# Kernel optimization log

Measured on AMD Instinct MI355X. Metric: run time of the kernel, lower is better.

The kernel has to match this reference:

```python
import jax, jax.numpy as jnp
import numpy as np

EMBED_DIM = 2048
HIDDEN_DIM = 2048
SEQ_LEN = 8192


def setup_inputs() -> dict:
    key = jax.random.key(0)
    ks = jax.random.split(key, 6)
    x = jax.random.normal(ks[0], (SEQ_LEN, EMBED_DIM), dtype=jnp.float32)
    # original uses torch.rand (uniform [0,1)) for params
    W_h = jax.random.uniform(ks[1], (HIDDEN_DIM, HIDDEN_DIM), dtype=jnp.float32)
    W_x = jax.random.uniform(ks[2], (HIDDEN_DIM, EMBED_DIM), dtype=jnp.float32)
    W_y = jax.random.uniform(ks[3], (EMBED_DIM, HIDDEN_DIM), dtype=jnp.float32)
    B_h = jax.random.uniform(ks[4], (HIDDEN_DIM,), dtype=jnp.float32)
    B_y = jax.random.uniform(ks[5], (EMBED_DIM,), dtype=jnp.float32)
    return {"x": x, "W_h": W_h, "W_x": W_x, "W_y": W_y, "B_h": B_h, "B_y": B_y}


def reference(x, W_h, W_x, W_y, B_h, B_y):
    # Precompute input projections for all timesteps in one GEMM: [T, H]
    xp = x @ W_x.T + B_h

    def step(h, xp_t):
        h_new = jnp.tanh(W_h @ h + xp_t)  # [H]
        return h_new, h_new

    h0 = jnp.zeros((W_h.shape[0],), dtype=x.dtype)
    h_final, hs = jax.lax.scan(step, h0, xp)  # hs: [T, H]
    # Output projection + softmax over embed dim, batched over timesteps
    logits = hs @ W_y.T + B_y  # [T, E]
    output = jax.nn.softmax(logits, axis=-1)
    return (h_final, output)
```

## Files before the change

kernel.cpp:

```cpp
#include <hip/hip_runtime.h>

#define T_SEQ 8192
#define HDIM  2048
#define EDIM  2048
#define RBLK  64
#define ROWS_PER_BLK (HDIM / RBLK)

typedef unsigned long long u64;
typedef __attribute__((ext_vector_type(4))) unsigned int u32x4;
typedef __attribute__((ext_vector_type(4))) float f32x4;

__device__ inline void poll_pair(const u64* p0, const u64* p1, u32x4& a, u32x4& b) {
    asm volatile("global_load_dwordx4 %0, %2, off sc1\n\t"
                 "global_load_dwordx4 %1, %3, off sc1\n\t"
                 "s_waitcnt vmcnt(0)"
                 : "=v"(a), "=v"(b) : "v"(p0), "v"(p1) : "memory");
}

__device__ inline f32x4 ld_w16(const float* p) {
    f32x4 r;
    asm volatile("global_load_dwordx4 %0, %1, off" : "=v"(r) : "v"(p));
    return r;
}

__device__ inline float fast_tanh(float z) {
    float zc = fminf(fmaxf(z, -15.f), 15.f);
    float zs = zc * 2.88539008177792681f;
    float ez; asm("v_exp_f32 %0, %1" : "=v"(ez) : "v"(zs));
    float rc; float ezp = ez + 1.f;
    asm("v_rcp_f32 %0, %1" : "=v"(rc) : "v"(ezp));
    return (ez - 1.f) * rc;
}

__global__ __launch_bounds__(256) void gemm128_nt_bias(
    const float* __restrict__ A, const float* __restrict__ B,
    const float* __restrict__ bias, float* __restrict__ C,
    int M, int N, int K)
{
    __shared__ float As[16][128 + 4];
    __shared__ float Bs[16][128 + 4];

    const int tid = threadIdx.x;
    const int tx = tid & 15;
    const int ty = tid >> 4;
    const int m0 = blockIdx.y * 128;
    const int n0 = blockIdx.x * 128;

    float acc[8][8] = {};

    for (int kk = 0; kk < K; kk += 16) {
        #pragma unroll
        for (int p = 0; p < 2; ++p) {
            int idx = p * 256 + tid;
            int r  = idx >> 2;
            int cb = (idx & 3) * 4;
            float4 va = *(const float4*)&A[(size_t)(m0 + r) * K + kk + cb];
            As[cb + 0][r] = va.x; As[cb + 1][r] = va.y;
            As[cb + 2][r] = va.z; As[cb + 3][r] = va.w;
            float4 vb = *(const float4*)&B[(size_t)(n0 + r) * K + kk + cb];
            Bs[cb + 0][r] = vb.x; Bs[cb + 1][r] = vb.y;
            Bs[cb + 2][r] = vb.z; Bs[cb + 3][r] = vb.w;
        }
        __syncthreads();
        #pragma unroll
        for (int k = 0; k < 16; ++k) {
            float4 a0 = *(const float4*)&As[k][ty * 8];
            float4 a1 = *(const float4*)&As[k][ty * 8 + 4];
            float4 b0 = *(const float4*)&Bs[k][tx * 8];
            float4 b1 = *(const float4*)&Bs[k][tx * 8 + 4];
            float av[8] = {a0.x, a0.y, a0.z, a0.w, a1.x, a1.y, a1.z, a1.w};
            float bv[8] = {b0.x, b0.y, b0.z, b0.w, b1.x, b1.y, b1.z, b1.w};
            #pragma unroll
            for (int i = 0; i < 8; ++i)
                #pragma unroll
                for (int j = 0; j < 8; ++j)
                    acc[i][j] = fmaf(av[i], bv[j], acc[i][j]);
        }
        __syncthreads();
    }

    float4 bb0 = *(const float4*)&bias[n0 + tx * 8];
    float4 bb1 = *(const float4*)&bias[n0 + tx * 8 + 4];
    float bv[8] = {bb0.x, bb0.y, bb0.z, bb0.w, bb1.x, bb1.y, bb1.z, bb1.w};
    #pragma unroll
    for (int i = 0; i < 8; ++i) {
        float4 o0, o1;
        o0.x = acc[i][0] + bv[0]; o0.y = acc[i][1] + bv[1];
        o0.z = acc[i][2] + bv[2]; o0.w = acc[i][3] + bv[3];
        o1.x = acc[i][4] + bv[4]; o1.y = acc[i][5] + bv[5];
        o1.z = acc[i][6] + bv[6]; o1.w = acc[i][7] + bv[7];
        float* cp = &C[(size_t)(m0 + ty * 8 + i) * N + n0 + tx * 8];
        *(float4*)cp = o0;
        *(float4*)(cp + 4) = o1;
    }
}

__global__ __launch_bounds__(256) void gemm128_nt_bias_tc(
    const float* __restrict__ A, const float* __restrict__ B,
    const float* __restrict__ bias, float* __restrict__ Ct,
    int M, int N, int K)
{
    __shared__ float As[16][128 + 4];
    __shared__ float Bs[16][128 + 4];

    const int tid = threadIdx.x;
    const int tx = tid & 15;
    const int ty = tid >> 4;
    const int m0 = blockIdx.y * 128;
    const int n0 = blockIdx.x * 128;

    float acc[8][8] = {};

    for (int kk = 0; kk < K; kk += 16) {
        #pragma unroll
        for (int p = 0; p < 2; ++p) {
            int idx = p * 256 + tid;
            int r  = idx >> 2;
            int cb = (idx & 3) * 4;
            float4 va = *(const float4*)&A[(size_t)(m0 + r) * K + kk + cb];
            As[cb + 0][r] = va.x; As[cb + 1][r] = va.y;
            As[cb + 2][r] = va.z; As[cb + 3][r] = va.w;
            float4 vb = *(const float4*)&B[(size_t)(n0 + r) * K + kk + cb];
            Bs[cb + 0][r] = vb.x; Bs[cb + 1][r] = vb.y;
            Bs[cb + 2][r] = vb.z; Bs[cb + 3][r] = vb.w;
        }
        __syncthreads();
        #pragma unroll
        for (int k = 0; k < 16; ++k) {
            float4 a0 = *(const float4*)&As[k][ty * 8];
            float4 a1 = *(const float4*)&As[k][ty * 8 + 4];
            float4 b0 = *(const float4*)&Bs[k][tx * 8];
            float4 b1 = *(const float4*)&Bs[k][tx * 8 + 4];
            float av[8] = {a0.x, a0.y, a0.z, a0.w, a1.x, a1.y, a1.z, a1.w};
            float bv[8] = {b0.x, b0.y, b0.z, b0.w, b1.x, b1.y, b1.z, b1.w};
            #pragma unroll
            for (int i = 0; i < 8; ++i)
                #pragma unroll
                for (int j = 0; j < 8; ++j)
                    acc[i][j] = fmaf(av[i], bv[j], acc[i][j]);
        }
        __syncthreads();
    }

    #pragma unroll
    for (int j = 0; j < 8; ++j) {
        float bb = bias[n0 + tx * 8 + j];
        float4 o0, o1;
        o0.x = acc[0][j] + bb; o0.y = acc[1][j] + bb;
        o0.z = acc[2][j] + bb; o0.w = acc[3][j] + bb;
        o1.x = acc[4][j] + bb; o1.y = acc[5][j] + bb;
        o1.z = acc[6][j] + bb; o1.w = acc[7][j] + bb;
        float* cp = &Ct[(size_t)(n0 + tx * 8 + j) * M + m0 + ty * 8];
        *(float4*)cp = o0;
        *(float4*)(cp + 4) = o1;
    }
}

__global__ __launch_bounds__(512, 1) void rnn_recurrence(
    const float* __restrict__ Wh, const float* __restrict__ xpT,
    float* __restrict__ Hs, u64* __restrict__ hbuf, int T)
{
    const int tid  = threadIdx.x;
    const int lane = tid & 63;
    const int wid  = tid >> 6;
    const int r0   = blockIdx.x * ROWS_PER_BLK + wid * 4;

    const float* wr0 = Wh + (size_t)(r0 + 0) * HDIM + lane * 4;
    const float* wr1 = Wh + (size_t)(r0 + 1) * HDIM + lane * 4;
    const float* wr2 = Wh + (size_t)(r0 + 2) * HDIM + lane * 4;
    const float* wr3 = Wh + (size_t)(r0 + 3) * HDIM + lane * 4;

    f32x4 w00 = ld_w16(wr0 + 0*256), w01 = ld_w16(wr0 + 1*256), w02 = ld_w16(wr0 + 2*256), w03 = ld_w16(wr0 + 3*256);
    f32x4 w04 = ld_w16(wr0 + 4*256), w05 = ld_w16(wr0 + 5*256), w06 = ld_w16(wr0 + 6*256), w07 = ld_w16(wr0 + 7*256);
    f32x4 w10 = ld_w16(wr1 + 0*256), w11 = ld_w16(wr1 + 1*256), w12 = ld_w16(wr1 + 2*256), w13 = ld_w16(wr1 + 3*256);
    f32x4 w14 = ld_w16(wr1 + 4*256), w15 = ld_w16(wr1 + 5*256), w16 = ld_w16(wr1 + 6*256), w17 = ld_w16(wr1 + 7*256);
    f32x4 w20 = ld_w16(wr2 + 0*256), w21 = ld_w16(wr2 + 1*256), w22 = ld_w16(wr2 + 2*256), w23 = ld_w16(wr2 + 3*256);
    f32x4 w24 = ld_w16(wr2 + 4*256), w25 = ld_w16(wr2 + 5*256), w26 = ld_w16(wr2 + 6*256), w27 = ld_w16(wr2 + 7*256);
    f32x4 w30 = ld_w16(wr3 + 0*256), w31 = ld_w16(wr3 + 1*256), w32 = ld_w16(wr3 + 2*256), w33 = ld_w16(wr3 + 3*256);
    f32x4 w34 = ld_w16(wr3 + 4*256), w35 = ld_w16(wr3 + 5*256), w36 = ld_w16(wr3 + 6*256), w37 = ld_w16(wr3 + 7*256);
    asm volatile("s_waitcnt vmcnt(0)" ::: "memory");

    __shared__ float hsm[HDIM];

    for (int t = 0; t < T; ++t) {
        float xq = 0.f;
        if (lane < 4) xq = xpT[(size_t)(r0 + lane) * T + t];

        float sv = 0.f;
        if (t > 0) {
            const u64* hb = hbuf + (size_t)(t & 1) * HDIM;
            const unsigned tg = (unsigned)t;
            const u64* p0 = hb + 2 * tid;
            const u64* p1 = hb + 1024 + 2 * tid;

            u32x4 a, b;
            poll_pair(p0, p1, a, b);
            while ((a.y != tg) | (a.w != tg) | (b.y != tg) | (b.w != tg))
                poll_pair(p0, p1, a, b);

            ((float2*)hsm)[tid] =
                make_float2(__uint_as_float(a.x), __uint_as_float(a.z));
            ((float2*)hsm)[tid + 512] =
                make_float2(__uint_as_float(b.x), __uint_as_float(b.z));
            __syncthreads();

            float s0 = 0.f, s1 = 0.f, s2 = 0.f, s3 = 0.f;
            #define RNN_STEP(IDX, WA, WB, WC, WD)                                   \
            {   float4 h4 = ((const float4*)hsm)[(IDX) * 64 + lane];                \
                s0 = fmaf(WA.x, h4.x, s0); s0 = fmaf(WA.y, h4.y, s0);               \
                s0 = fmaf(WA.z, h4.z, s0); s0 = fmaf(WA.w, h4.w, s0);               \
                s1 = fmaf(WB.x, h4.x, s1); s1 = fmaf(WB.y, h4.y, s1);               \
                s1 = fmaf(WB.z, h4.z, s1); s1 = fmaf(WB.w, h4.w, s1);               \
                s2 = fmaf(WC.x, h4.x, s2); s2 = fmaf(WC.y, h4.y, s2);               \
                s2 = fmaf(WC.z, h4.z, s2); s2 = fmaf(WC.w, h4.w, s2);               \
                s3 = fmaf(WD.x, h4.x, s3); s3 = fmaf(WD.y, h4.y, s3);               \
                s3 = fmaf(WD.z, h4.z, s3); s3 = fmaf(WD.w, h4.w, s3); }
            RNN_STEP(0, w00, w10, w20, w30)
            RNN_STEP(1, w01, w11, w21, w31)
            RNN_STEP(2, w02, w12, w22, w32)
            RNN_STEP(3, w03, w13, w23, w33)
            RNN_STEP(4, w04, w14, w24, w34)
            RNN_STEP(5, w05, w15, w25, w35)
            RNN_STEP(6, w06, w16, w26, w36)
            RNN_STEP(7, w07, w17, w27, w37)
            #undef RNN_STEP

            float fa = (lane & 1) ? s1 : s0;
            float fb = (lane & 1) ? s0 : s1;
            fa += __shfl_xor(fb, 1);
            float fc = (lane & 1) ? s3 : s2;
            float fd = (lane & 1) ? s2 : s3;
            fc += __shfl_xor(fd, 1);
            float fe = (lane & 2) ? fc : fa;
            float ff = (lane & 2) ? fa : fc;
            fe += __shfl_xor(ff, 2);
            #pragma unroll
            for (int off = 4; off < 64; off <<= 1) fe += __shfl_xor(fe, off);
            sv = fe;
        }

        if (lane < 4) {
            float hn = fast_tanh(sv + xq);
            u64 pk = ((u64)(unsigned)(t + 1) << 32) | (u64)__float_as_uint(hn);
            (void)__hip_atomic_exchange(
                &hbuf[(size_t)((t + 1) & 1) * HDIM + r0 + lane], pk,
                __ATOMIC_RELAXED, __HIP_MEMORY_SCOPE_AGENT);
            Hs[(size_t)t * HDIM + r0 + lane] = hn;
        }
    }
}

__global__ __launch_bounds__(256) void softmax_rows(
    const float* __restrict__ logits, float* __restrict__ out)
{
    const int row = blockIdx.x;
    const float4* in4 = (const float4*)(logits + (size_t)row * EDIM);
    float4* out4 = (float4*)(out + (size_t)row * EDIM);

    float4 v0 = in4[threadIdx.x];
    float4 v1 = in4[threadIdx.x + 256];

    float m = fmaxf(fmaxf(fmaxf(v0.x, v0.y), fmaxf(v0.z, v0.w)),
                    fmaxf(fmaxf(v1.x, v1.y), fmaxf(v1.z, v1.w)));
    #pragma unroll
    for (int off = 32; off > 0; off >>= 1) m = fmaxf(m, __shfl_xor(m, off));

    __shared__ float red[4];
    if ((threadIdx.x & 63) == 0) red[threadIdx.x >> 6] = m;
    __syncthreads();
    m = fmaxf(fmaxf(red[0], red[1]), fmaxf(red[2], red[3]));
    __syncthreads();

    float e[8];
    e[0] = expf(v0.x - m); e[1] = expf(v0.y - m);
    e[2] = expf(v0.z - m); e[3] = expf(v0.w - m);
    e[4] = expf(v1.x - m); e[5] = expf(v1.y - m);
    e[6] = expf(v1.z - m); e[7] = expf(v1.w - m);

    float s = e[0] + e[1] + e[2] + e[3] + e[4] + e[5] + e[6] + e[7];
    #pragma unroll
    for (int off = 32; off > 0; off >>= 1) s += __shfl_xor(s, off);
    if ((threadIdx.x & 63) == 0) red[threadIdx.x >> 6] = s;
    __syncthreads();
    s = red[0] + red[1] + red[2] + red[3];

    float inv = 1.0f / s;
    out4[threadIdx.x]       = make_float4(e[0] * inv, e[1] * inv, e[2] * inv, e[3] * inv);
    out4[threadIdx.x + 256] = make_float4(e[4] * inv, e[5] * inv, e[6] * inv, e[7] * inv);
}

__global__ void copy_vec(const float* __restrict__ src, float* __restrict__ dst, int n)
{
    int i = blockIdx.x * blockDim.x + threadIdx.x;
    if (i < n) dst[i] = src[i];
}

extern "C" void kernel_launch(void* const* d_in, const int* in_sizes, int n_in,
                              void* d_out, int out_size, void* d_ws, size_t ws_size,
                              hipStream_t stream)
{
    const float* x  = (const float*)d_in[0];
    const float* Wh = (const float*)d_in[1];
    const float* Wx = (const float*)d_in[2];
    const float* Wy = (const float*)d_in[3];
    const float* Bh = (const float*)d_in[4];
    const float* By = (const float*)d_in[5];

    float* out    = (float*)d_out;
    float* hfinal = out;
    float* hs     = out + HDIM;

    float* xpT  = (float*)d_ws;
    u64*   hbuf = (u64*)((char*)d_ws + (size_t)T_SEQ * HDIM * 4);
    float* logits = xpT;

    hipMemsetAsync(hbuf, 0, 2 * HDIM * sizeof(u64), stream);

    gemm128_nt_bias_tc<<<dim3(HDIM / 128, T_SEQ / 128), 256, 0, stream>>>(
        x, Wx, Bh, xpT, T_SEQ, HDIM, EDIM);

    int T = T_SEQ;
    const float* xpT_c = xpT;
    void* args[] = {(void*)&Wh, (void*)&xpT_c, (void*)&hs, (void*)&hbuf, (void*)&T};
    hipLaunchCooperativeKernel((void*)rnn_recurrence, dim3(RBLK), dim3(512),
                               args, 0, stream);

    gemm128_nt_bias<<<dim3(EDIM / 128, T_SEQ / 128), 256, 0, stream>>>(
        hs, Wy, By, logits, T_SEQ, EDIM, HDIM);

    copy_vec<<<dim3(HDIM / 256), 256, 0, stream>>>(
        hs + (size_t)(T_SEQ - 1) * HDIM, hfinal, HDIM);

    softmax_rows<<<dim3(T_SEQ), 256, 0, stream>>>(logits, hs);
}
```

Before: 14.34 ms.

## Fuse output projection into recurrence kernel and drop separate logits GEMM

The recurrence kernel now also computes each timestep's output logits. After each step it dots the previous hidden state, already staged in a double-buffered shared array, against rows of W_y read from global memory. A tail block handles the final timestep. This removes the separate output-projection GEMM, the hidden-state store and reload, and the copy kernel; softmax then runs in place on the output buffer. The cost is that every step streams the full W_y (16 MB across all blocks) from cache or memory inside the latency-critical sequential loop, which may lengthen each step. The change also leaves behind an unused macro.

```diff
diff --git a/kernel.cpp b/kernel.cpp
--- a/kernel.cpp
+++ b/kernel.cpp
@@ -32,9 +32,9 @@
     return (ez - 1.f) * rc;
 }
 
-__global__ __launch_bounds__(256) void gemm128_nt_bias(
+__global__ __launch_bounds__(256) void gemm128_nt_bias_tc(
     const float* __restrict__ A, const float* __restrict__ B,
-    const float* __restrict__ bias, float* __restrict__ C,
+    const float* __restrict__ bias, float* __restrict__ Ct,
     int M, int N, int K)
 {
     __shared__ float As[16][128 + 4];
@@ -79,69 +79,6 @@
         __syncthreads();
     }
 
-    float4 bb0 = *(const float4*)&bias[n0 + tx * 8];
-    float4 bb1 = *(const float4*)&bias[n0 + tx * 8 + 4];
-    float bv[8] = {bb0.x, bb0.y, bb0.z, bb0.w, bb1.x, bb1.y, bb1.z, bb1.w};
-    #pragma unroll
-    for (int i = 0; i < 8; ++i) {
-        float4 o0, o1;
-        o0.x = acc[i][0] + bv[0]; o0.y = acc[i][1] + bv[1];
-        o0.z = acc[i][2] + bv[2]; o0.w = acc[i][3] + bv[3];
-        o1.x = acc[i][4] + bv[4]; o1.y = acc[i][5] + bv[5];
-        o1.z = acc[i][6] + bv[6]; o1.w = acc[i][7] + bv[7];
-        float* cp = &C[(size_t)(m0 + ty * 8 + i) * N + n0 + tx * 8];
-        *(float4*)cp = o0;
-        *(float4*)(cp + 4) = o1;
-    }
-}
-
-__global__ __launch_bounds__(256) void gemm128_nt_bias_tc(
-    const float* __restrict__ A, const float* __restrict__ B,
-    const float* __restrict__ bias, float* __restrict__ Ct,
-    int M, int N, int K)
-{
-    __shared__ float As[16][128 + 4];
-    __shared__ float Bs[16][128 + 4];
-
-    const int tid = threadIdx.x;
-    const int tx = tid & 15;
-    const int ty = tid >> 4;
-    const int m0 = blockIdx.y * 128;
-    const int n0 = blockIdx.x * 128;
-
-    float acc[8][8] = {};
-
-    for (int kk = 0; kk < K; kk += 16) {
-        #pragma unroll
-        for (int p = 0; p < 2; ++p) {
-            int idx = p * 256 + tid;
-            int r  = idx >> 2;
-            int cb = (idx & 3) * 4;
-            float4 va = *(const float4*)&A[(size_t)(m0 + r) * K + kk + cb];
-            As[cb + 0][r] = va.x; As[cb + 1][r] = va.y;
-            As[cb + 2][r] = va.z; As[cb + 3][r] = va.w;
-            float4 vb = *(const float4*)&B[(size_t)(n0 + r) * K + kk + cb];
-            Bs[cb + 0][r] = vb.x; Bs[cb + 1][r] = vb.y;
-            Bs[cb + 2][r] = vb.z; Bs[cb + 3][r] = vb.w;
-        }
-        __syncthreads();
-        #pragma unroll
-        for (int k = 0; k < 16; ++k) {
-            float4 a0 = *(const float4*)&As[k][ty * 8];
-            float4 a1 = *(const float4*)&As[k][ty * 8 + 4];
-            float4 b0 = *(const float4*)&Bs[k][tx * 8];
-            float4 b1 = *(const float4*)&Bs[k][tx * 8 + 4];
-            float av[8] = {a0.x, a0.y, a0.z, a0.w, a1.x, a1.y, a1.z, a1.w};
-            float bv[8] = {b0.x, b0.y, b0.z, b0.w, b1.x, b1.y, b1.z, b1.w};
-            #pragma unroll
-            for (int i = 0; i < 8; ++i)
-                #pragma unroll
-                for (int j = 0; j < 8; ++j)
-                    acc[i][j] = fmaf(av[i], bv[j], acc[i][j]);
-        }
-        __syncthreads();
-    }
-
     #pragma unroll
     for (int j = 0; j < 8; ++j) {
         float bb = bias[n0 + tx * 8 + j];
@@ -157,8 +94,10 @@
 }
 
 __global__ __launch_bounds__(512, 1) void rnn_recurrence(
-    const float* __restrict__ Wh, const float* __restrict__ xpT,
-    float* __restrict__ Hs, u64* __restrict__ hbuf, int T)
+    const float* __restrict__ Wh, const float* __restrict__ Wy,
+    const float* __restrict__ By, const float* __restrict__ xpT,
+    float* __restrict__ hfinal, float* __restrict__ logits,
+    u64* __restrict__ hbuf, int T)
 {
     const int tid  = threadIdx.x;
     const int lane = tid & 63;
@@ -180,7 +119,28 @@
     f32x4 w34 = ld_w16(wr3 + 4*256), w35 = ld_w16(wr3 + 5*256), w36 = ld_w16(wr3 + 6*256), w37 = ld_w16(wr3 + 7*256);
     asm volatile("s_waitcnt vmcnt(0)" ::: "memory");
 
-    __shared__ float hsm[HDIM];
+    const float* wy0 = Wy + (size_t)(r0 + 0) * HDIM + lane * 4;
+    const float* wy1 = Wy + (size_t)(r0 + 1) * HDIM + lane * 4;
+    const float* wy2 = Wy + (size_t)(r0 + 2) * HDIM + lane * 4;
+    const float* wy3 = Wy + (size_t)(r0 + 3) * HDIM + lane * 4;
+    const float byq = (lane < 4) ? By[r0 + lane] : 0.f;
+
+    __shared__ float hsm[2][HDIM];
+
+    #define WH_DOT(HP)                                                          \
+        float s0 = 0.f, s1 = 0.f, s2 = 0.f, s3 = 0.f;                           \
+        {                                                                       \
+        _Pragma("unroll")                                                       \
+        for (int t8 = 0; t8 < 8; ++t8) {                                        \
+            float4 h4 = ((const float4*)(HP))[t8 * 64 + lane];                  \
+            const f32x4* wp = (t8==0)? &w00 : (t8==1)? &w01 : (t8==2)? &w02 :   \
+                              (t8==3)? &w03 : (t8==4)? &w04 : (t8==5)? &w05 :   \
+                              (t8==6)? &w06 : &w07;                             \
+            (void)wp;                                                           \
+        }                                                                       \
+        }
+
+    #undef WH_DOT
 
     for (int t = 0; t < T; ++t) {
         float xq = 0.f;
@@ -198,15 +158,16 @@
             while ((a.y != tg) | (a.w != tg) | (b.y != tg) | (b.w != tg))
                 poll_pair(p0, p1, a, b);
 
-            ((float2*)hsm)[tid] =
+            float* hp = hsm[t & 1];
+            ((float2*)hp)[tid] =
                 make_float2(__uint_as_float(a.x), __uint_as_float(a.z));
-            ((float2*)hsm)[tid + 512] =
+            ((float2*)hp)[tid + 512] =
                 make_float2(__uint_as_float(b.x), __uint_as_float(b.z));
             __syncthreads();
 
             float s0 = 0.f, s1 = 0.f, s2 = 0.f, s3 = 0.f;
             #define RNN_STEP(IDX, WA, WB, WC, WD)                                   \
-            {   float4 h4 = ((const float4*)hsm)[(IDX) * 64 + lane];                \
+            {   float4 h4 = ((const float4*)hp)[(IDX) * 64 + lane];                 \
                 s0 = fmaf(WA.x, h4.x, s0); s0 = fmaf(WA.y, h4.y, s0);               \
                 s0 = fmaf(WA.z, h4.z, s0); s0 = fmaf(WA.w, h4.w, s0);               \
                 s1 = fmaf(WB.x, h4.x, s1); s1 = fmaf(WB.y, h4.y, s1);               \
@@ -239,14 +200,98 @@
             sv = fe;
         }
 
+        float hn = fast_tanh(sv + xq);
         if (lane < 4) {
-            float hn = fast_tanh(sv + xq);
             u64 pk = ((u64)(unsigned)(t + 1) << 32) | (u64)__float_as_uint(hn);
             (void)__hip_atomic_exchange(
                 &hbuf[(size_t)((t + 1) & 1) * HDIM + r0 + lane], pk,
                 __ATOMIC_RELAXED, __HIP_MEMORY_SCOPE_AGENT);
-            Hs[(size_t)t * HDIM + r0 + lane] = hn;
-        }
+            if (t == T - 1) hfinal[r0 + lane] = hn;
+        }
+
+        if (t > 0) {
+            const float* hp = hsm[t & 1];
+            float q0 = 0.f, q1 = 0.f, q2 = 0.f, q3 = 0.f;
+            #pragma unroll
+            for (int t8 = 0; t8 < 8; ++t8) {
+                float4 h4 = ((const float4*)hp)[t8 * 64 + lane];
+                float4 y0 = *(const float4*)(wy0 + t8 * 256);
+                float4 y1 = *(const float4*)(wy1 + t8 * 256);
+                float4 y2 = *(const float4*)(wy2 + t8 * 256);
+                float4 y3 = *(const float4*)(wy3 + t8 * 256);
+                q0 = fmaf(y0.x, h4.x, q0); q0 = fmaf(y0.y, h4.y, q0);
+                q0 = fmaf(y0.z, h4.z, q0); q0 = fmaf(y0.w, h4.w, q0);
+                q1 = fmaf(y1.x, h4.x, q1); q1 = fmaf(y1.y, h4.y, q1);
+                q1 = fmaf(y1.z, h4.z, q1); q1 = fmaf(y1.w, h4.w, q1);
+                q2 = fmaf(y2.x, h4.x, q2); q2 = fmaf(y2.y, h4.y, q2);
+                q2 = fmaf(y2.z, h4.z, q2); q2 = fmaf(y2.w, h4.w, q2);
+                q3 = fmaf(y3.x, h4.x, q3); q3 = fmaf(y3.y, h4.y, q3);
+                q3 = fmaf(y3.z, h4.z, q3); q3 = fmaf(y3.w, h4.w, q3);
+            }
+            float ga = (lane & 1) ? q1 : q0;
+            float gb = (lane & 1) ? q0 : q1;
+            ga += __shfl_xor(gb, 1);
+            float gc = (lane & 1) ? q3 : q2;
+            float gd = (lane & 1) ? q2 : q3;
+            gc += __shfl_xor(gd, 1);
+            float ge = (lane & 2) ? gc : ga;
+            float gf = (lane & 2) ? ga : gc;
+            ge += __shfl_xor(gf, 2);
+            #pragma unroll
+            for (int off = 4; off < 64; off <<= 1) ge += __shfl_xor(ge, off);
+            if (lane < 4)
+                logits[(size_t)(t - 1) * EDIM + r0 + lane] = ge + byq;
+        }
+    }
+
+    {
+        const u64* hb = hbuf + (size_t)(T & 1) * HDIM;
+        const unsigned tg = (unsigned)T;
+        const u64* p0 = hb + 2 * tid;
+        const u64* p1 = hb + 1024 + 2 * tid;
+
+        u32x4 a, b;
+        poll_pair(p0, p1, a, b);
+        while ((a.y != tg) | (a.w != tg) | (b.y != tg) | (b.w != tg))
+            poll_pair(p0, p1, a, b);
+
+        float* hp = hsm[T & 1];
+        ((float2*)hp)[tid] =
+            make_float2(__uint_as_float(a.x), __uint_as_float(a.z));
+        ((float2*)hp)[tid + 512] =
+            make_float2(__uint_as_float(b.x), __uint_as_float(b.z));
+        __syncthreads();
+
+        float q0 = 0.f, q1 = 0.f, q2 = 0.f, q3 = 0.f;
+        #pragma unroll
+        for (int t8 = 0; t8 < 8; ++t8) {
+            float4 h4 = ((const float4*)hp)[t8 * 64 + lane];
+            float4 y0 = *(const float4*)(wy0 + t8 * 256);
+            float4 y1 = *(const float4*)(wy1 + t8 * 256);
+            float4 y2 = *(const float4*)(wy2 + t8 * 256);
+            float4 y3 = *(const float4*)(wy3 + t8 * 256);
+            q0 = fmaf(y0.x, h4.x, q0); q0 = fmaf(y0.y, h4.y, q0);
+            q0 = fmaf(y0.z, h4.z, q0); q0 = fmaf(y0.w, h4.w, q0);
+            q1 = fmaf(y1.x, h4.x, q1); q1 = fmaf(y1.y, h4.y, q1);
+            q1 = fmaf(y1.z, h4.z, q1); q1 = fmaf(y1.w, h4.w, q1);
+            q2 = fmaf(y2.x, h4.x, q2); q2 = fmaf(y2.y, h4.y, q2);
+            q2 = fmaf(y2.z, h4.z, q2); q2 = fmaf(y2.w, h4.w, q2);
+            q3 = fmaf(y3.x, h4.x, q3); q3 = fmaf(y3.y, h4.y, q3);
+            q3 = fmaf(y3.z, h4.z, q3); q3 = fmaf(y3.w, h4.w, q3);
+        }
+        float ga = (lane & 1) ? q1 : q0;
+        float gb = (lane & 1) ? q0 : q1;
+        ga += __shfl_xor(gb, 1);
+        float gc = (lane & 1) ? q3 : q2;
+        float gd = (lane & 1) ? q2 : q3;
+        gc += __shfl_xor(gd, 1);
+        float ge = (lane & 2) ? gc : ga;
+        float gf = (lane & 2) ? ga : gc;
+        ge += __shfl_xor(gf, 2);
+        #pragma unroll
+        for (int off = 4; off < 64; off <<= 1) ge += __shfl_xor(ge, off);
+        if (lane < 4)
+            logits[(size_t)(T - 1) * EDIM + r0 + lane] = ge + byq;
     }
 }
 
@@ -287,12 +332,6 @@
     float inv = 1.0f / s;
     out4[threadIdx.x]       = make_float4(e[0] * inv, e[1] * inv, e[2] * inv, e[3] * inv);
     out4[threadIdx.x + 256] = make_float4(e[4] * inv, e[5] * inv, e[6] * inv, e[7] * inv);
-}
-
-__global__ void copy_vec(const float* __restrict__ src, float* __restrict__ dst, int n)
-{
-    int i = blockIdx.x * blockDim.x + threadIdx.x;
-    if (i < n) dst[i] = src[i];
 }
 
 extern "C" void kernel_launch(void* const* d_in, const int* in_sizes, int n_in,
@@ -308,11 +347,10 @@
 
     float* out    = (float*)d_out;
     float* hfinal = out;
-    float* hs     = out + HDIM;
+    float* logits = out + HDIM;
 
     float* xpT  = (float*)d_ws;
     u64*   hbuf = (u64*)((char*)d_ws + (size_t)T_SEQ * HDIM * 4);
-    float* logits = xpT;
 
     hipMemsetAsync(hbuf, 0, 2 * HDIM * sizeof(u64), stream);
 
@@ -320,16 +358,12 @@
         x, Wx, Bh, xpT, T_SEQ, HDIM, EDIM);
 
     int T = T_SEQ;
+    const float* Wh_c = Wh; const float* Wy_c = Wy; const float* By_c = By;
     const float* xpT_c = xpT;
-    void* args[] = {(void*)&Wh, (void*)&xpT_c, (void*)&hs, (void*)&hbuf, (void*)&T};
+    void* args[] = {(void*)&Wh_c, (void*)&Wy_c, (void*)&By_c, (void*)&xpT_c,
+                    (void*)&hfinal, (void*)&logits, (void*)&hbuf, (void*)&T};
     hipLaunchCooperativeKernel((void*)rnn_recurrence, dim3(RBLK), dim3(512),
                                args, 0, stream);
 
-    gemm128_nt_bias<<<dim3(EDIM / 128, T_SEQ / 128), 256, 0, stream>>>(
-        hs, Wy, By, logits, T_SEQ, EDIM, HDIM);
-
-    copy_vec<<<dim3(HDIM / 256), 256, 0, stream>>>(
-        hs + (size_t)(T_SEQ - 1) * HDIM, hfinal, HDIM);
-
-    softmax_rows<<<dim3(T_SEQ), 256, 0, stream>>>(logits, hs);
-}
+    softmax_rows<<<dim3(T_SEQ), 256, 0, stream>>>(logits, logits);
+}
```

Result: slower. 35.29 ms (+146.1%).
